# Kernel optimization log

Measured on AMD Instinct MI355X. Metric: run time of the kernel, lower is better.

The kernel has to match this reference:

```python
import jax, jax.numpy as jnp
import numpy as np

# Hyperparameters matching the torch module instantiation
STRIDE = (2, 2, 2)
PADDING = (1, 1, 1)
OUTPUT_PADDING = (1, 1, 1)
DILATION = (2, 2, 2)
KERNEL = (3, 3, 3)


def setup_inputs() -> dict:
    key = jax.random.key(0)
    k1, k2, k3 = jax.random.split(key, 3)
    x = jax.random.normal(k1, (2, 64, 32, 32, 32), dtype=jnp.float32)
    # torch ConvTranspose3d weight layout: (C_in, C_out//groups, kD, kH, kW)
    weight = jax.random.normal(k2, (64, 32, 3, 3, 3), dtype=jnp.float32) * 0.05
    bias = jax.random.normal(k3, (32,), dtype=jnp.float32) * 0.05
    return {"x": x, "weight": weight, "bias": bias}


def reference(x, weight, bias):
    # Same math as the naive torch module: zero-insertion upsample by stride,
    # symmetric pad by dilation*(k-1)-padding, dense conv3d with the spatially
    # flipped weight at rhs dilation, trailing output_padding, then bias add.
    # lhs_dilation performs the zero-insertion implicitly (identical result).
    pad = tuple(max(0, d * (k - 1) - p)
                for d, k, p in zip(DILATION, KERNEL, PADDING))
    # (C_in, C_out, k,k,k) -> (C_out, C_in, k,k,k), flipped spatially
    w = jnp.flip(jnp.transpose(weight, (1, 0, 2, 3, 4)), axis=(2, 3, 4))
    out = jax.lax.conv_general_dilated(
        x, w,
        window_strides=(1, 1, 1),
        padding=[(p, p) for p in pad],
        lhs_dilation=STRIDE,
        rhs_dilation=DILATION,
        dimension_numbers=("NCDHW", "OIDHW", "NCDHW"),
    )
    opd, oph, opw = OUTPUT_PADDING
    out = jnp.pad(out, ((0, 0), (0, 0), (0, opd), (0, oph), (0, opw)))
    return out + bias[None, :, None, None, None]
```

## Files before the change

kernel.cpp:

```cpp
#include <hip/hip_runtime.h>


#define DOUT 66
#define PL (DOUT*DOUT)
#define ROW_B 4352
#define SLOT_B 17408

typedef _Float16 half8   __attribute__((ext_vector_type(8)));
typedef float    floatx16 __attribute__((ext_vector_type(16)));
typedef float    floatx4  __attribute__((ext_vector_type(4)));
typedef float    floatx2  __attribute__((ext_vector_type(2)));

__global__ void __launch_bounds__(256) wprep(const float* __restrict__ w,
                                             _Float16* __restrict__ wA)
{
    int o = blockIdx.x * 256 + threadIdx.x;
    int j = o & 7;
    int tmp = o >> 3;
    int lane = tmp & 63;
    int g = tmp >> 6;
    int cc = g / 27, tap = g - cc * 27;
    int co = lane & 31, khalf = lane >> 5;
    int ci = cc * 16 + khalf * 8 + j;
    wA[o] = (_Float16)w[ci * 864 + co * 27 + tap];
}

__global__ void __launch_bounds__(256, 2) convt(
    const float* __restrict__ x, const _Float16* __restrict__ wA,
    const float* __restrict__ bias, float* __restrict__ out)
{
    __shared__ __align__(16) unsigned char xlds[4 * SLOT_B];

    const int tid  = threadIdx.x;
    const int lane = tid & 63;
    const int wv   = tid >> 6;

    unsigned b = blockIdx.x;
    const unsigned xcd = b & 7u;
    const int n   = (int)(xcd & 1u);
    const unsigned rest = b >> 3;
    const int hq2   = (int)(rest & 3u);
    const int dpair = (int)(rest >> 2);
    const int hpg = (int)((xcd >> 1) * 4 + hq2);
    const int hpb = hpg * 2;
    const int dp0 = dpair * 2;

    const float* xn = x + (size_t)n * 2097152;
    const int gq  = tid & 7;
    const int ccg = (tid >> 3) & 7;
    const int ihl = wv;
    const int ih  = hpb - 1 + ihl;
    const bool ihok = (unsigned)ih < 32u;

    auto stage = [&](int slot, int id) {
        unsigned char* dst = xlds + slot * SLOT_B + ihl * ROW_B
                           + ccg * 544 + (gq * 4 + 1) * 16;
        if (ihok & ((unsigned)id < 32u)) {
            const float* src = xn + ccg * 262144 + (id * 32 + ih) * 32 + gq * 4;
            floatx4 f[8];
            #pragma unroll
            for (int j = 0; j < 8; ++j) f[j] = *(const floatx4*)(src + j * 32768);
            #pragma unroll
            for (int m = 0; m < 4; ++m) {
                unsigned p0 = __builtin_bit_cast(unsigned,
                    __builtin_amdgcn_cvt_pkrtz(f[0][m], f[1][m]));
                unsigned p1 = __builtin_bit_cast(unsigned,
                    __builtin_amdgcn_cvt_pkrtz(f[2][m], f[3][m]));
                unsigned p2 = __builtin_bit_cast(unsigned,
                    __builtin_amdgcn_cvt_pkrtz(f[4][m], f[5][m]));
                unsigned p3 = __builtin_bit_cast(unsigned,
                    __builtin_amdgcn_cvt_pkrtz(f[6][m], f[7][m]));
                *(uint4*)(dst + m * 16) = make_uint4(p0, p1, p2, p3);
            }
        } else {
            #pragma unroll
            for (int m = 0; m < 4; ++m)
                *(uint4*)(dst + m * 16) = make_uint4(0, 0, 0, 0);
        }
        if (tid < 64) {
            const int r2 = tid >> 4, rem = tid & 15;
            const int cg = rem >> 1, side = rem & 1;
            *(uint4*)(xlds + slot * SLOT_B + r2 * ROW_B + cg * 544
                      + (side ? 33 * 16 : 0)) = make_uint4(0, 0, 0, 0);
        }
    };

    floatx4 pf[8];
    bool pfv = false;
    auto pf_load = [&](int id) {
        pfv = ihok & ((unsigned)id < 32u);
        if (pfv) {
            const float* src = xn + ccg * 262144 + (id * 32 + ih) * 32 + gq * 4;
            #pragma unroll
            for (int j = 0; j < 8; ++j) pf[j] = *(const floatx4*)(src + j * 32768);
        }
    };
    auto pf_write = [&](int slot) {
        unsigned char* dst = xlds + slot * SLOT_B + ihl * ROW_B
                           + ccg * 544 + (gq * 4 + 1) * 16;
        if (pfv) {
            #pragma unroll
            for (int m = 0; m < 4; ++m) {
                unsigned p0 = __builtin_bit_cast(unsigned,
                    __builtin_amdgcn_cvt_pkrtz(pf[0][m], pf[1][m]));
                unsigned p1 = __builtin_bit_cast(unsigned,
                    __builtin_amdgcn_cvt_pkrtz(pf[2][m], pf[3][m]));
                unsigned p2 = __builtin_bit_cast(unsigned,
                    __builtin_amdgcn_cvt_pkrtz(pf[4][m], pf[5][m]));
                unsigned p3 = __builtin_bit_cast(unsigned,
                    __builtin_amdgcn_cvt_pkrtz(pf[6][m], pf[7][m]));
                *(uint4*)(dst + m * 16) = make_uint4(p0, p1, p2, p3);
            }
        } else {
            #pragma unroll
            for (int m = 0; m < 4; ++m)
                *(uint4*)(dst + m * 16) = make_uint4(0, 0, 0, 0);
        }
        if (tid < 64) {
            const int r2 = tid >> 4, rem = tid & 15;
            const int cg = rem >> 1, side = rem & 1;
            *(uint4*)(xlds + slot * SLOT_B + r2 * ROW_B + cg * 544
                      + (side ? 33 * 16 : 0)) = make_uint4(0, 0, 0, 0);
        }
    };

    uint4 A[27];
    const _Float16* wl = wA + ((size_t)wv * 27 * 64 + lane) * 8;
    #pragma unroll
    for (int t = 0; t < 27; ++t) A[t] = *(const uint4*)(wl + t * 512);

    const int wp    = lane & 31;
    const int khalf = lane >> 5;
    const int cbase = (2 * wv + khalf) * 544 + wp * 16;

    float bv[16];
    #pragma unroll
    for (int r = 0; r < 16; ++r)
        bv[r] = bias[(r & 3) + 8 * (r >> 2) + 4 * khalf];

    stage(0, dp0 - 1);
    stage(1, dp0);
    stage(2, dp0 + 1);
    __syncthreads();

    auto mfma_unit = [&](int base, floatx16& a0, floatx16& a1) {
        #pragma unroll
        for (int kd = 0; kd < 3; ++kd)
        #pragma unroll
        for (int kh = 0; kh < 3; ++kh)
        #pragma unroll
        for (int kw = 0; kw < 3; ++kw) {
            const int tap = (kd * 3 + kh) * 3 + kw;
            const uint4* bp0 = (const uint4*)(xlds + (base + 2 - kd) * SLOT_B
                               + (2 - kh) * ROW_B + cbase + (2 - kw) * 16);
            a0 = __builtin_amdgcn_mfma_f32_32x32x16_f16(
                __builtin_bit_cast(half8, A[tap]),
                __builtin_bit_cast(half8, bp0[0]), a0, 0, 0, 0);
            const uint4* bp1 = (const uint4*)((const char*)bp0 + ROW_B);
            acc1_step:
            a1 = __builtin_amdgcn_mfma_f32_32x32x16_f16(
                __builtin_bit_cast(half8, A[tap]),
                __builtin_bit_cast(half8, bp1[0]), a1, 0, 0, 0);
        }
    };

    auto reduce_store = [&](int u, int dp, floatx16& a0, floatx16& a1) {
        float* part = (float*)(xlds + u * SLOT_B);
        const int od = 2 * dp + 1;

        __syncthreads();
        if (wv != 0) {
            #pragma unroll
            for (int r = 0; r < 16; ++r)
                part[(wv - 1) * 1024 + r * 64 + lane] = a0[r];
        }
        __syncthreads();
        float s[16];
        if (wv == 0) {
            #pragma unroll
            for (int r = 0; r < 16; ++r)
                s[r] = a0[r] + part[r * 64 + lane]
                             + part[1024 + r * 64 + lane]
                             + part[2048 + r * 64 + lane];
        }
        __syncthreads();
        if (wv != 1) {
            const int idx = (wv == 0) ? 0 : (wv - 1);
            #pragma unroll
            for (int r = 0; r < 16; ++r)
                part[idx * 1024 + r * 64 + lane] = a1[r];
        }
        if (wv == 0) {
            const int oh = 2 * hpb + 1;
            #pragma unroll
            for (int r = 0; r < 16; ++r) {
                const int co = (r & 3) + 8 * (r >> 2) + 4 * khalf;
                floatx2* orow = (floatx2*)(out +
                    ((size_t)(n * 32 + co) * DOUT + od) * PL + oh * DOUT);
                floatx2 vv = {bv[r], s[r] + bv[r]};
                __builtin_nontemporal_store(vv, orow + wp);
                if (wp == 31) {
                    floatx2 bb = {bv[r], bv[r]};
                    __builtin_nontemporal_store(bb, orow + 32);
                }
            }
        }
        __syncthreads();
        if (wv == 1) {
            float s1[16];
            #pragma unroll
            for (int r = 0; r < 16; ++r)
                s1[r] = a1[r] + part[r * 64 + lane]
                              + part[1024 + r * 64 + lane]
                              + part[2048 + r * 64 + lane];
            const int oh = 2 * hpb + 3;
            #pragma unroll
            for (int r = 0; r < 16; ++r) {
                const int co = (r & 3) + 8 * (r >> 2) + 4 * khalf;
                floatx2* orow = (floatx2*)(out +
                    ((size_t)(n * 32 + co) * DOUT + od) * PL + oh * DOUT);
                floatx2 vv = {bv[r], s1[r] + bv[r]};
                __builtin_nontemporal_store(vv, orow + wp);
                if (wp == 31) {
                    floatx2 bb = {bv[r], bv[r]};
                    __builtin_nontemporal_store(bb, orow + 32);
                }
            }
        } else if (wv >= 2) {
            const bool tails = (hpg == 15);
            const bool extra = (dp == 31);
            const int ohA = (wv == 2) ? 2 * hpb : 2 * hpb + 2;
            const int ohT = (wv == 2) ? 64 : 65;
            const int e0  = 4 * hpg + ((wv == 2) ? 0 : 2);
            auto putrow = [&](float* plane, int oh, floatx2 bb) {
                floatx2* rw = (floatx2*)(plane + oh * DOUT);
                __builtin_nontemporal_store(bb, rw + wp);
                if (wp == 31) __builtin_nontemporal_store(bb, rw + 32);
            };
            #pragma unroll
            for (int r = 0; r < 16; ++r) {
                const int co = (r & 3) + 8 * (r >> 2) + 4 * khalf;
                const floatx2 bb = {bv[r], bv[r]};
                float* pc    = out + (size_t)(n * 32 + co) * ((size_t)DOUT * PL);
                float* podd  = pc + (size_t)od * PL;
                float* peven = pc + (size_t)(od - 1) * PL;
                putrow(podd, ohA, bb);
                if (tails) putrow(podd, ohT, bb);
                putrow(peven, e0, bb);
                putrow(peven, e0 + 1, bb);
                if (tails) putrow(peven, ohT, bb);
                if (extra) {
                    float* p64 = pc + (size_t)64 * PL;
                    float* p65 = pc + (size_t)65 * PL;
                    putrow(p64, e0, bb);
                    putrow(p64, e0 + 1, bb);
                    putrow(p65, e0, bb);
                    putrow(p65, e0 + 1, bb);
                    if (tails) { putrow(p64, ohT, bb); putrow(p65, ohT, bb); }
                }
            }
        }
    };

    {
        floatx16 a0 = {}, a1 = {};
        pf_load(dp0 + 2);
        mfma_unit(0, a0, a1);
        pf_write(3);
        reduce_store(0, dp0, a0, a1);
    }
    {
        floatx16 a0 = {}, a1 = {};
        mfma_unit(1, a0, a1);
        reduce_store(1, dp0 + 1, a0, a1);
    }
}

extern "C" void kernel_launch(void* const* d_in, const int* in_sizes, int n_in,
                              void* d_out, int out_size, void* d_ws, size_t ws_size,
                              hipStream_t stream) {
    const float* x    = (const float*)d_in[0];
    const float* wgt  = (const float*)d_in[1];
    const float* bias = (const float*)d_in[2];
    float* out = (float*)d_out;
    _Float16* wA = (_Float16*)d_ws;

    wprep<<<216, 256, 0, stream>>>(wgt, wA);
    convt<<<512, 256, 0, stream>>>(x, wA, bias, out);
}
```

Measured before the change: 126.2 us.

## Stage conv results in LDS and write output as contiguous float4 row spans

The reduced accumulators are now placed into an LDS value table instead of being written straight to global memory as scattered float2 pairs. All threads then write contiguous multi-row spans of each output plane as float4 stores, interleaving bias-only and computed positions. Planes holding only bias (even depth) are filled up front as contiguous float4 spans, overlapping with staging. The goal is better-coalesced, wider writes to the large output, at the cost of an extra LDS pass, more barriers, per-element index arithmetic, and dropping the nontemporal store hints.

```diff
diff --git a/kernel.cpp b/kernel.cpp
--- a/kernel.cpp
+++ b/kernel.cpp
@@ -9,7 +9,6 @@
 typedef _Float16 half8   __attribute__((ext_vector_type(8)));
 typedef float    floatx16 __attribute__((ext_vector_type(16)));
 typedef float    floatx4  __attribute__((ext_vector_type(4)));
-typedef float    floatx2  __attribute__((ext_vector_type(2)));
 
 __global__ void __launch_bounds__(256) wprep(const float* __restrict__ w,
                                              _Float16* __restrict__ wA)
@@ -52,6 +51,9 @@
     const int ih  = hpb - 1 + ihl;
     const bool ihok = (unsigned)ih < 32u;
 
+    const int co_s = tid >> 3;
+    const int l8   = tid & 7;
+
     auto stage = [&](int slot, int id) {
         unsigned char* dst = xlds + slot * SLOT_B + ihl * ROW_B
                            + ccg * 544 + (gq * 4 + 1) * 16;
@@ -133,14 +135,37 @@
     const int khalf = lane >> 5;
     const int cbase = (2 * wv + khalf) * 544 + wp * 16;
 
-    float bv[16];
-    #pragma unroll
-    for (int r = 0; r < 16; ++r)
-        bv[r] = bias[(r & 3) + 8 * (r >> 2) + 4 * khalf];
+    const float bvc = bias[co_s];
+    const int nr    = (hpg == 15) ? 6 : 4;
+    const int npass = (hpg == 15) ? 13 : 9;
+    const int SP    = nr * 66 / 4;
+
+    auto bias_span = [&](float* base) {
+        const floatx4 bb = {bvc, bvc, bvc, bvc};
+        for (int p = 0; p < npass; ++p) {
+            const int q = l8 + 8 * p;
+            if (q < SP) *(floatx4*)(base + 4 * q) = bb;
+        }
+    };
 
     stage(0, dp0 - 1);
     stage(1, dp0);
     stage(2, dp0 + 1);
+
+    {
+        #pragma unroll
+        for (int u = 0; u < 2; ++u) {
+            float* pb = out + ((size_t)(n * 32 + co_s) * DOUT + 2 * (dp0 + u)) * PL
+                        + 4 * hpg * DOUT;
+            bias_span(pb);
+        }
+        if (dp0 == 30) {
+            float* p64 = out + ((size_t)(n * 32 + co_s) * DOUT + 64) * PL
+                         + 4 * hpg * DOUT;
+            bias_span(p64);
+            bias_span(p64 + PL);
+        }
+    }
     __syncthreads();
 
     auto mfma_unit = [&](int base, floatx16& a0, floatx16& a1) {
@@ -157,108 +182,80 @@
                 __builtin_bit_cast(half8, A[tap]),
                 __builtin_bit_cast(half8, bp0[0]), a0, 0, 0, 0);
             const uint4* bp1 = (const uint4*)((const char*)bp0 + ROW_B);
-            acc1_step:
             a1 = __builtin_amdgcn_mfma_f32_32x32x16_f16(
                 __builtin_bit_cast(half8, A[tap]),
                 __builtin_bit_cast(half8, bp1[0]), a1, 0, 0, 0);
         }
     };
 
-    auto reduce_store = [&](int u, int dp, floatx16& a0, floatx16& a1) {
-        float* part = (float*)(xlds + u * SLOT_B);
-        const int od = 2 * dp + 1;
-
+    auto reduce_val = [&](int u, floatx16& a0, floatx16& a1) {
+        float* scratch = (float*)(xlds + u * SLOT_B);
+        float* val0    = (float*)(xlds + u * SLOT_B + 12288);
+        float* val1    = scratch;
         __syncthreads();
         if (wv != 0) {
             #pragma unroll
             for (int r = 0; r < 16; ++r)
-                part[(wv - 1) * 1024 + r * 64 + lane] = a0[r];
-        }
-        __syncthreads();
-        float s[16];
+                scratch[(wv - 1) * 1024 + r * 64 + lane] = a0[r];
+        }
+        __syncthreads();
         if (wv == 0) {
             #pragma unroll
+            for (int r = 0; r < 16; ++r) {
+                float s = a0[r] + scratch[r * 64 + lane]
+                                + scratch[1024 + r * 64 + lane]
+                                + scratch[2048 + r * 64 + lane];
+                const int co = (r & 3) + 8 * (r >> 2) + 4 * khalf;
+                val0[co * 33 + wp] = s;
+            }
+        }
+        __syncthreads();
+        if (wv != 1) {
+            const int idx = (wv == 0) ? 0 : wv - 1;
+            #pragma unroll
             for (int r = 0; r < 16; ++r)
-                s[r] = a0[r] + part[r * 64 + lane]
-                             + part[1024 + r * 64 + lane]
-                             + part[2048 + r * 64 + lane];
-        }
-        __syncthreads();
-        if (wv != 1) {
-            const int idx = (wv == 0) ? 0 : (wv - 1);
+                scratch[idx * 1024 + r * 64 + lane] = a1[r];
+        }
+        __syncthreads();
+        if (wv == 1) {
+            float s[16];
             #pragma unroll
             for (int r = 0; r < 16; ++r)
-                part[idx * 1024 + r * 64 + lane] = a1[r];
-        }
-        if (wv == 0) {
-            const int oh = 2 * hpb + 1;
+                s[r] = a1[r] + scratch[r * 64 + lane]
+                             + scratch[1024 + r * 64 + lane]
+                             + scratch[2048 + r * 64 + lane];
             #pragma unroll
             for (int r = 0; r < 16; ++r) {
                 const int co = (r & 3) + 8 * (r >> 2) + 4 * khalf;
-                floatx2* orow = (floatx2*)(out +
-                    ((size_t)(n * 32 + co) * DOUT + od) * PL + oh * DOUT);
-                floatx2 vv = {bv[r], s[r] + bv[r]};
-                __builtin_nontemporal_store(vv, orow + wp);
-                if (wp == 31) {
-                    floatx2 bb = {bv[r], bv[r]};
-                    __builtin_nontemporal_store(bb, orow + 32);
+                val1[co * 33 + wp] = s[r];
+            }
+        }
+        __syncthreads();
+    };
+
+    auto store_A = [&](int u, int dp) {
+        const float* val0 = (const float*)(xlds + u * SLOT_B + 12288);
+        const float* val1 = (const float*)(xlds + u * SLOT_B);
+        float* base = out + ((size_t)(n * 32 + co_s) * DOUT + 2 * dp + 1) * PL
+                      + 4 * hpg * DOUT;
+        for (int p = 0; p < npass; ++p) {
+            const int q = l8 + 8 * p;
+            if (q >= SP) continue;
+            floatx4 o;
+            #pragma unroll
+            for (int j = 0; j < 4; ++j) {
+                const int e = 4 * q + j;
+                const int rl = (e >= 330) ? 5 : (e >= 264) ? 4 : (e >= 198) ? 3 :
+                               (e >= 132) ? 2 : (e >= 66) ? 1 : 0;
+                const int ow = e - rl * 66;
+                float v = bvc;
+                if ((rl == 1 || rl == 3) && (ow & 1) && ow < 65) {
+                    const float* vt = (rl == 1) ? val0 : val1;
+                    v += vt[co_s * 33 + (ow >> 1)];
                 }
-            }
-        }
-        __syncthreads();
-        if (wv == 1) {
-            float s1[16];
-            #pragma unroll
-            for (int r = 0; r < 16; ++r)
-                s1[r] = a1[r] + part[r * 64 + lane]
-                              + part[1024 + r * 64 + lane]
-                              + part[2048 + r * 64 + lane];
-            const int oh = 2 * hpb + 3;
-            #pragma unroll
-            for (int r = 0; r < 16; ++r) {
-                const int co = (r & 3) + 8 * (r >> 2) + 4 * khalf;
-                floatx2* orow = (floatx2*)(out +
-                    ((size_t)(n * 32 + co) * DOUT + od) * PL + oh * DOUT);
-                floatx2 vv = {bv[r], s1[r] + bv[r]};
-                __builtin_nontemporal_store(vv, orow + wp);
-                if (wp == 31) {
-                    floatx2 bb = {bv[r], bv[r]};
-                    __builtin_nontemporal_store(bb, orow + 32);
-                }
-            }
-        } else if (wv >= 2) {
-            const bool tails = (hpg == 15);
-            const bool extra = (dp == 31);
-            const int ohA = (wv == 2) ? 2 * hpb : 2 * hpb + 2;
-            const int ohT = (wv == 2) ? 64 : 65;
-            const int e0  = 4 * hpg + ((wv == 2) ? 0 : 2);
-            auto putrow = [&](float* plane, int oh, floatx2 bb) {
-                floatx2* rw = (floatx2*)(plane + oh * DOUT);
-                __builtin_nontemporal_store(bb, rw + wp);
-                if (wp == 31) __builtin_nontemporal_store(bb, rw + 32);
-            };
-            #pragma unroll
-            for (int r = 0; r < 16; ++r) {
-                const int co = (r & 3) + 8 * (r >> 2) + 4 * khalf;
-                const floatx2 bb = {bv[r], bv[r]};
-                float* pc    = out + (size_t)(n * 32 + co) * ((size_t)DOUT * PL);
-                float* podd  = pc + (size_t)od * PL;
-                float* peven = pc + (size_t)(od - 1) * PL;
-                putrow(podd, ohA, bb);
-                if (tails) putrow(podd, ohT, bb);
-                putrow(peven, e0, bb);
-                putrow(peven, e0 + 1, bb);
-                if (tails) putrow(peven, ohT, bb);
-                if (extra) {
-                    float* p64 = pc + (size_t)64 * PL;
-                    float* p65 = pc + (size_t)65 * PL;
-                    putrow(p64, e0, bb);
-                    putrow(p64, e0 + 1, bb);
-                    putrow(p65, e0, bb);
-                    putrow(p65, e0 + 1, bb);
-                    if (tails) { putrow(p64, ohT, bb); putrow(p65, ohT, bb); }
-                }
-            }
+                o[j] = v;
+            }
+            *(floatx4*)(base + 4 * q) = o;
         }
     };
 
@@ -267,12 +264,14 @@
         pf_load(dp0 + 2);
         mfma_unit(0, a0, a1);
         pf_write(3);
-        reduce_store(0, dp0, a0, a1);
+        reduce_val(0, a0, a1);
+        store_A(0, dp0);
     }
     {
         floatx16 a0 = {}, a1 = {};
         mfma_unit(1, a0, a1);
-        reduce_store(1, dp0 + 1, a0, a1);
+        reduce_val(1, a0, a1);
+        store_A(1, dp0 + 1);
     }
 }
 
```

Result: faster. 107.6 us (-14.7%).
